# Kernel optimization log

Hardware: AMD Instinct MI355X
Metric: run time of the kernel (lower is better)

Reference implementation:

```python
import jax, jax.numpy as jnp
import numpy as np

TOPK = 13
NUM_CLASSES = 80
ALPHA = 1.0
BETA = 3.0
EPS = 1e-9
K_NEAR = 4
N_BINS = 36  # theta bins: arange(0, 360, 10)


def _dist_max_per_bin(anc_points, gt_pts):
    """gt_pts: (bs,nm,360,2), anc_points: (na,2) -> (bs,nm,na,36) ray targets."""
    d = gt_pts[:, :, None, :, :] - anc_points[None, None, :, None, :]  # (bs,nm,na,360,2)
    dist = jnp.sqrt(jnp.sum(d * d, axis=-1))                           # (bs,nm,na,360)
    ang = jnp.rad2deg(jnp.arctan2(d[..., 1], d[..., 0])) % 360.0       # (bs,nm,na,360)
    theta = jnp.arange(0, 360, 360 // N_BINS).astype(ang.dtype)        # (36,)

    def per_theta(th):
        diff = jnp.abs(ang - th)
        diff = jnp.where(diff > 180.0, 360.0 - diff, diff)
        neg_v, idx = jax.lax.top_k(-diff, K_NEAR)   # 4 nearest-angle contour pts
        val = -neg_v
        dk = jnp.take_along_axis(dist, idx, axis=-1)
        dk = jnp.where(jnp.min(val, axis=-1, keepdims=True) > 3.0, 1e-6, dk)
        return jnp.max(dk, axis=-1)                 # (bs,nm,na)

    dm = jax.lax.map(per_theta, theta)              # (36,bs,nm,na); chunked to bound memory
    return jnp.maximum(jnp.moveaxis(dm, 0, -1), 1e-6)


def _mask_iou(target, pred):
    l_max = jnp.maximum(target, pred)
    l_min = jnp.maximum(jnp.minimum(target, pred), 1e-6)
    return jnp.sum(l_min, -1) / jnp.sum(l_max, -1)


def _forward(pd_scores, pd_bboxes, anc_points, gt_labels, gt_bboxes, mask_gt, gt_coor):
    bs, na, nc = pd_scores.shape
    nm = gt_bboxes.shape[1]
    gl = gt_labels[..., 0]            # (bs,nm) int
    mgt = mask_gt[..., 0]             # (bs,nm) float
    gt_pts = gt_coor.reshape(bs, nm, 360, 2)

    # select_candidates_in_gts: anchor center strictly inside gt box
    lt, rb = gt_bboxes[..., :2], gt_bboxes[..., 2:]
    deltas = jnp.concatenate([anc_points[None, None] - lt[:, :, None],
                              rb[:, :, None] - anc_points[None, None]], axis=-1)
    mask_in_gts = (jnp.min(deltas, -1) > 1e-9).astype(pd_scores.dtype)  # (bs,nm,na)
    mask_sel = (mask_in_gts * mgt[:, :, None]) > 0

    # get_box_metrics_polar (dense over (bs,nm,na) instead of boolean-mask select)
    dist_max = _dist_max_per_bin(anc_points, gt_pts)                    # (bs,nm,na,36)
    overlaps = jnp.where(mask_sel, _mask_iou(dist_max, pd_bboxes[:, None]), 0.0)
    bbox_scores = jnp.take_along_axis(jnp.swapaxes(pd_scores, 1, 2), gl[:, :, None], axis=1)
    bbox_scores = jnp.where(mask_sel, bbox_scores, 0.0)
    align_metric = (bbox_scores ** ALPHA) * (overlaps ** BETA)

    # select_topk_candidates
    _, topk_idxs = jax.lax.top_k(align_metric, TOPK)
    topk_idxs = jnp.where(mgt[:, :, None] > 0, topk_idxs, 0)
    count = jnp.sum(jax.nn.one_hot(topk_idxs, na, dtype=align_metric.dtype), axis=-2)
    mask_topk = jnp.where(count > 1, 0.0, count)
    mask_pos = mask_topk * mask_in_gts * mgt[:, :, None]

    # select_highest_overlaps
    fg = jnp.sum(mask_pos, -2)                                          # (bs,na)
    multi = fg[:, None, :] > 1
    is_max = jnp.moveaxis(jax.nn.one_hot(jnp.argmax(overlaps, 1), nm, dtype=mask_pos.dtype), -1, 1)
    mask_pos = jnp.where(multi, is_max, mask_pos)
    fg_mask = jnp.sum(mask_pos, -2)
    target_gt_idx = jnp.argmax(mask_pos, -2)                            # (bs,na)

    # per-positive ray-distance targets + polar centerness (dense, masked)
    mask_pos_b = mask_pos > 0
    gt_dist = jnp.where(mask_pos_b[..., None], dist_max, 0.0)           # (bs,nm,na,36)
    cent = jnp.sqrt(jnp.min(dist_max, -1) / jnp.max(dist_max, -1))
    centerness_gt = jnp.where(mask_pos_b, cent, 0.0)                    # (bs,nm,na)

    # get_targets
    target_labels = jnp.maximum(jnp.take_along_axis(gl, target_gt_idx, axis=1), 0)
    target_bboxes = jnp.take_along_axis(gt_bboxes, target_gt_idx[..., None], axis=1)
    target_scores = jax.nn.one_hot(target_labels, NUM_CLASSES, dtype=pd_scores.dtype)
    target_scores = jnp.where((fg_mask > 0)[..., None], target_scores, 0.0)

    am = align_metric * mask_pos
    pos_align = jnp.max(am, -1, keepdims=True)
    pos_ov = jnp.max(overlaps * mask_pos, -1, keepdims=True)
    norm_align = jnp.max(am * pos_ov / (pos_align + EPS), -2)[..., None]  # (bs,na,1)
    target_scores = target_scores * norm_align

    return (target_labels, target_bboxes, target_scores, mask_pos_b,
            target_gt_idx, gt_dist, centerness_gt, fg_mask > 0)


def setup_inputs():
    key = jax.random.key(0)
    k = jax.random.split(key, 6)
    bs, nc, nm = 2, 80, 10
    pts, strs = [], []
    for s in (8, 16, 32):  # 640x640 YOLO grid -> 8400 anchors
        n = 640 // s
        yv, xv = np.meshgrid(np.arange(n), np.arange(n), indexing='ij')
        pts.append(np.stack([(xv + 0.5) * s, (yv + 0.5) * s], -1).reshape(-1, 2))
        strs.append(np.full((pts[-1].shape[0], 1), s, dtype=np.float32))
    anc_points = jnp.asarray(np.concatenate(pts).astype(np.float32))
    stride_tensor = jnp.asarray(np.concatenate(strs))
    na = anc_points.shape[0]
    pd_scores = jax.random.uniform(k[0], (bs, na, nc), dtype=jnp.float32)
    pd_bboxes = jax.random.uniform(k[1], (bs, na, 36), dtype=jnp.float32) * 100.0 + 1.0
    gt_labels = jax.random.randint(k[2], (bs, nm, 1), 0, nc)
    ctr = jax.random.uniform(k[3], (bs, nm, 2), dtype=jnp.float32) * 440.0 + 100.0
    wh = jax.random.uniform(k[4], (bs, nm, 2), dtype=jnp.float32) * 140.0 + 40.0
    gt_bboxes = jnp.concatenate([ctr - wh / 2.0, ctr + wh / 2.0], -1)
    th = jnp.arange(360.0) * (jnp.pi / 180.0)
    rad = (jnp.min(wh, -1, keepdims=True) / 2.0) * (0.6 + 0.4 * jax.random.uniform(k[5], (bs, nm, 360), dtype=jnp.float32))
    ray = jnp.stack([jnp.cos(th), jnp.sin(th)], -1)  # (360,2)
    gt_coor = (ctr[:, :, None, :] + rad[..., None] * ray[None, None]).reshape(bs, nm, 720)
    mask_gt = jnp.ones((bs, nm, 1), dtype=jnp.float32).at[1, 7:].set(0.0)
    return dict(pd_scores=pd_scores, pd_bboxes=pd_bboxes, anc_points=anc_points,
                gt_labels=gt_labels, gt_bboxes=gt_bboxes, mask_gt=mask_gt,
                gt_coor=gt_coor, stride_tensor=stride_tensor, ss=640,
                gt_center=ctr, imgsz=640)


def reference(pd_scores, pd_bboxes, anc_points, gt_labels, gt_bboxes, mask_gt, gt_coor, stride_tensor, ss, gt_center, imgsz):
    # ss, gt_center, imgsz, stride_tensor are accepted (as in the torch signature) but unused
    return _forward(pd_scores, pd_bboxes, anc_points, gt_labels, gt_bboxes, mask_gt, gt_coor)
```

## Files before the change

### kernel.cpp

```cpp
#include <hip/hip_runtime.h>

#define BS 2
#define NM 10
#define NA 8400
#define NC 80
#define NBIN 36
#define KTOP 13
#define NRECT (BS*NM*3)
#define WDIST_CAP 16384

typedef unsigned long long ull;

__device__ __forceinline__ void rect_one(int bm, int lv,
    const float* __restrict__ gtb, const float* __restrict__ mgt,
    int& x0, int& y0, int& cx, int& cy, int& cnt, int& n, int& base){
  cnt = 0; x0 = 0; y0 = 0; cx = 0; cy = 0; n = 0; base = 0;
  if (mgt[bm] > 0.f){
    float s = (float)(8 << lv);
    n = 640 >> (3 + lv);
    base = (lv == 0) ? 0 : ((lv == 1) ? 6400 : 8000);
    float lx = gtb[bm*4+0], ly = gtb[bm*4+1];
    float rx = gtb[bm*4+2], ry = gtb[bm*4+3];
    int a0 = (int)ceilf(lx/s - 0.5f); a0 = min(max(a0, 0), n);
    while (a0 > 0   &&  (((a0-1)+0.5f)*s - lx > 1e-9f)) a0--;
    while (a0 < n   && !(((a0  )+0.5f)*s - lx > 1e-9f)) a0++;
    int a1 = (int)floorf(rx/s - 0.5f); a1 = min(max(a1, -1), n-1);
    while (a1 < n-1 &&  (rx - ((a1+1)+0.5f)*s > 1e-9f)) a1++;
    while (a1 >= 0  && !(rx - ((a1  )+0.5f)*s > 1e-9f)) a1--;
    int b0 = (int)ceilf(ly/s - 0.5f); b0 = min(max(b0, 0), n);
    while (b0 > 0   &&  (((b0-1)+0.5f)*s - ly > 1e-9f)) b0--;
    while (b0 < n   && !(((b0  )+0.5f)*s - ly > 1e-9f)) b0++;
    int b1 = (int)floorf(ry/s - 0.5f); b1 = min(max(b1, -1), n-1);
    while (b1 < n-1 &&  (ry - ((b1+1)+0.5f)*s > 1e-9f)) b1++;
    while (b1 >= 0  && !(ry - ((b1  )+0.5f)*s > 1e-9f)) b1--;
    cx = max(0, a1 - a0 + 1);
    cy = max(0, b1 - b0 + 1);
    cnt = cx * cy;
    x0 = a0; y0 = b0;
  }
}

__device__ __forceinline__ void rect_setup(int tid,
    const float* __restrict__ gtb, const float* __restrict__ mgt,
    int* sx0, int* sy0, int* scx, int* scy, int* scum, int* sn, int* sbase){
  if (tid < NRECT){
    int bm = tid/3, lv = tid - bm*3;
    int x0, y0, cx, cy, cnt, n, base;
    rect_one(bm, lv, gtb, mgt, x0, y0, cx, cy, cnt, n, base);
    sx0[tid] = x0; sy0[tid] = y0; scx[tid] = cx; scy[tid] = cy;
    scum[tid] = cnt; sn[tid] = n; sbase[tid] = base;
  }
  __syncthreads();
  if (tid < 64){
    int c = (tid < NRECT) ? scum[tid] : 0;
    int incl = c;
#pragma unroll
    for (int st = 1; st < 64; st <<= 1){
      int o = __shfl_up(incl, st);
      if (tid >= st) incl += o;
    }
    if (tid < NRECT) scum[tid] = incl - c;
    if (tid == NRECT-1) scum[NRECT] = incl;
  }
  __syncthreads();
}

__device__ __forceinline__ int pair_from_p(int p,
    const int* sx0, const int* sy0, const int* scx,
    const int* scum, const int* sn, const int* sbase){
  int lo = 0, hi = NRECT - 1;
  while (lo < hi){ int mid = (lo + hi + 1) >> 1; if (scum[mid] <= p) lo = mid; else hi = mid - 1; }
  int r = lo;
  int idx = p - scum[r];
  int cx = scx[r];
  int yi = idx / cx;
  int xi = idx - yi*cx;
  int a = sbase[r] + (sy0[r] + yi)*sn[r] + (sx0[r] + xi);
  int bm = r/3;
  return bm*NA + a;
}

__device__ __forceinline__ ull shflx_u64(ull v, int off){
  unsigned lo = (unsigned)v, hi = (unsigned)(v >> 32);
  lo = __shfl_xor(lo, off); hi = __shfl_xor(hi, off);
  return ((ull)hi << 32) | lo;
}

__global__ __launch_bounds__(128)
void k_dist(const float* __restrict__ pds, const float* __restrict__ pdb,
            const float* __restrict__ anc, const int* __restrict__ gl,
            const float* __restrict__ gtb, const float* __restrict__ mgt,
            const float* __restrict__ coor,
            float* __restrict__ out, float* __restrict__ wf){
  float* o_labels  = out;
  float* o_bboxes  = o_labels + BS*NA;
  float* o_scores  = o_bboxes + BS*NA*4;
  float* o_maskpos = o_scores + (size_t)BS*NA*NC;
  float* o_gtidx   = o_maskpos + BS*NM*NA;
  float* o_gtdist  = o_gtidx + BS*NA;
  float* o_cent    = o_gtdist + (size_t)BS*NM*NA*NBIN;
  float* o_fg      = o_cent + BS*NM*NA;

  float* w_align = wf + 16;
  float* w_ovl   = w_align + BS*NM*NA;
  float* w_dist  = w_ovl + BS*NM*NA;

  __shared__ int sx0[NRECT], sy0[NRECT], scx[NRECT], scy[NRECT], scum[NRECT+1], sn[NRECT], sbase[NRECT];
  __shared__ float4 s_ad[360];
  __shared__ int s_cnt[NBIN], s_off[NBIN+1], s_cur[NBIN];
  __shared__ int s_fbl[NBIN];
  __shared__ int s_nfb;

  int tid = threadIdx.x;
  int lane = tid & 63, wave = tid >> 6;

  rect_setup(tid, gtb, mgt, sx0, sy0, scx, scy, scum, sn, sbase);
  int total = scum[NRECT];

  {
    int gtid = blockIdx.x*128 + tid, gsz = gridDim.x*128;
    float4 z4 = make_float4(0.f,0.f,0.f,0.f);
    float4* zs = (float4*)o_scores;
    for (int i = gtid; i < (BS*NA*NC)/4; i += gsz) zs[i] = z4;
    float4* zg = (float4*)o_gtdist;
    for (int i = gtid; i < (BS*NM*NA*NBIN)/4; i += gsz) zg[i] = z4;
    float4* zc = (float4*)o_cent;
    for (int i = gtid; i < (BS*NM*NA)/4; i += gsz) zc[i] = z4;
    float4* zm = (float4*)o_maskpos;
    for (int i = gtid; i < (BS*NM*NA)/4; i += gsz) zm[i] = z4;
    if (gtid < 16) wf[gtid] = 0.f;
    for (int t = gtid; t < BS*NA; t += gsz){
      int b = t / NA;
      o_gtidx[t] = 0.f;
      o_fg[t] = 0.f;
      int lbl = gl[b*NM]; if (lbl < 0) lbl = 0;
      o_labels[t] = (float)lbl;
      const float* bx = gtb + (b*NM)*4;
      ((float4*)o_bboxes)[t] = make_float4(bx[0], bx[1], bx[2], bx[3]);
    }
    for (int row = gtid; row < BS*NM*NA; row += gsz){
      int bm = row / NA;
      int a  = row - bm*NA;
      int lv = (a < 6400) ? 0 : ((a < 8000) ? 1 : 2);
      int ai = a - ((lv == 0) ? 0 : ((lv == 1) ? 6400 : 8000));
      int r = bm*3 + lv;
      bool inrect = false;
      if (scx[r] > 0 && scy[r] > 0){
        int n = sn[r];
        int y = ai / n, x = ai - y*n;
        inrect = (x >= sx0[r] && x < sx0[r]+scx[r] &&
                  y >= sy0[r] && y < sy0[r]+scy[r]);
      }
      if (!inrect) w_ovl[row] = 0.f;
    }
  }

  if (tid < NBIN) s_cnt[tid] = 0;
  if (tid == 0) s_nfb = 0;
  __syncthreads();

  for (int p = blockIdx.x; p < total; p += gridDim.x){
    int t = pair_from_p(p, sx0, sy0, scx, scum, sn, sbase);
    int a = t % NA; int bm = t / NA; int b = bm / NM;
    float ax = anc[2*a], ay = anc[2*a+1];
    const float2* cc2 = (const float2*)(coor + bm*720);

    float pr = 0.f, sc = 0.f;
    if (wave == 0){
      if (lane < NBIN) pr = pdb[((size_t)b*NA + a)*NBIN + lane];
      int cls = gl[bm];
      sc = pds[((size_t)b*NA + a)*NC + cls];
    }

    float anR[3], diR[3]; int buR[3];
#pragma unroll
    for (int r = 0; r < 3; r++){
      int i = tid + r*128;
      buR[r] = -1;
      if (i < 360){
        float2 cxy = cc2[i];
        float dx = cxy.x - ax;
        float dy = cxy.y - ay;
        diR[r] = sqrtf(dx*dx + dy*dy);
        float an = atan2f(dy, dx) * 57.29577951308232f;
        if (an < 0.f) an += 360.f;
        anR[r] = an;
        int bu = min((int)(an * 0.1f), NBIN-1);
        buR[r] = bu;
        atomicAdd(&s_cnt[bu], 1);
      }
    }
    __syncthreads();

    if (wave == 0){
      int c = (lane < NBIN) ? s_cnt[lane] : 0;
      int incl = c;
#pragma unroll
      for (int st = 1; st < 64; st <<= 1){
        int o = __shfl_up(incl, st);
        if (lane >= st) incl += o;
      }
      if (lane < NBIN){ s_off[lane+1] = incl; s_cur[lane] = incl - c; }
      if (lane == 0) s_off[0] = 0;
    }
    __syncthreads();

    if (tid < NBIN) s_cnt[tid] = 0;
#pragma unroll
    for (int r = 0; r < 3; r++){
      if (buR[r] >= 0){
        int pos = atomicAdd(&s_cur[buR[r]], 1);
        s_ad[pos] = make_float4(anR[r], diR[r], (float)(tid + r*128), 0.f);
      }
    }
    __syncthreads();

#define EVALJ(J, TH) { \
      float4 ad = s_ad[J]; \
      unsigned int ixv = (unsigned int)(int)ad.z; \
      float df = fabsf(ad.x - (TH)); \
      df = fminf(df, 360.f - df); \
      ull key = ((ull)__float_as_uint(df) << 32) | ixv; \
      if (key < k3){ \
        k3 = key; d3 = ad.y; \
        if (k3 < k2){ ull tk=k2; k2=k3; k3=tk; float td=d2; d2=d3; d3=td; } \
        if (k2 < k1){ ull tk=k1; k1=k2; k2=tk; float td=d1; d1=d2; d2=td; } \
        if (k1 < k0){ ull tk=k0; k0=k1; k1=tk; float td=d0; d0=d1; d1=td; } \
      } }

    if (wave == 0){
      float dfin = 1e-6f;
      bool act = (lane < NBIN);
      bool need_fb = false;
      if (act){
        float th = (float)(lane*10);
        int r0s, r0e, r1s, r1e;
        if (lane == 0)      { r0s = s_off[35]; r0e = s_off[36]; r1s = 0; r1e = s_off[2]; }
        else if (lane == 35){ r0s = s_off[34]; r0e = s_off[36]; r1s = 0; r1e = s_off[1]; }
        else                { r0s = s_off[lane-1]; r0e = s_off[lane+2]; r1s = 0; r1e = 0; }
        ull k0,k1,k2,k3; float d0,d1,d2,d3;
        k0=k1=k2=k3=~0ull; d0=d1=d2=d3=0.f;
        for (int j = r0s; j < r0e; j++) EVALJ(j, th)
        for (int j = r1s; j < r1e; j++) EVALJ(j, th)
        float v0m = __uint_as_float((unsigned)(k0 >> 32));
        float d4v = __uint_as_float((unsigned)(k3 >> 32));
        if (!(v0m <= 3.0f)){
          dfin = 1e-6f;
        } else if (!(d4v <= 9.99f)){
          int fi = atomicAdd(&s_nfb, 1);
          s_fbl[fi] = lane;
          need_fb = true;
        } else {
          dfin = fmaxf(fmaxf(fmaxf(d0,d1),fmaxf(d2,d3)), 1e-6f);
        }
      }
      int nfb = s_nfb;
      for (int f = 0; f < nfb; f++){
        int fb = s_fbl[f];
        float th = (float)(fb*10);
        ull k0,k1,k2,k3; float d0,d1,d2,d3;
        k0=k1=k2=k3=~0ull; d0=d1=d2=d3=0.f;
        for (int j = lane; j < 360; j += 64){
          EVALJ(j, th)
        }
        ull hk = k0; float hd = d0; int hp = 0;
        float dmax = 0.f;
#pragma unroll
        for (int r = 0; r < 4; r++){
          ull mk = hk; float md = hd;
#pragma unroll
          for (int off = 1; off < 64; off <<= 1){
            ull ok = shflx_u64(mk, off);
            float od = __shfl_xor(md, off);
            if (ok < mk){ mk = ok; md = od; }
          }
          if (hk == mk){
            hp++;
            hk = (hp==1)? k1 : (hp==2)? k2 : (hp==3)? k3 : ~0ull;
            hd = (hp==1)? d1 : (hp==2)? d2 : (hp==3)? d3 : 0.f;
          }
          dmax = fmaxf(dmax, md);
        }
        if (lane == fb && need_fb) dfin = fmaxf(dmax, 1e-6f);
      }
      if (lane == 0) s_nfb = 0;

      float sum_min = 0.f, sum_max = 0.f;
      if (act){
        if (p < WDIST_CAP) w_dist[(size_t)p*NBIN + lane] = dfin;
        sum_max = fmaxf(dfin, pr);
        sum_min = fmaxf(fminf(dfin, pr), 1e-6f);
      }
      for (int off = 32; off > 0; off >>= 1){
        sum_min += __shfl_down(sum_min, off);
        sum_max += __shfl_down(sum_max, off);
      }
      if (lane == 0){
        float ov = sum_min / sum_max;
        w_align[t] = sc * ov * ov * ov;
        w_ovl[t]   = ov;
      }
    }
#undef EVALJ
    __syncthreads();
  }
}

__global__ __launch_bounds__(256)
void k_tail(const float* __restrict__ gtb, const float* __restrict__ mgt,
            const float* __restrict__ w_align, const float* __restrict__ w_ovl,
            const float* __restrict__ w_dist, const int* __restrict__ gl,
            float* __restrict__ o_labels, float* __restrict__ o_bboxes,
            float* __restrict__ o_maskpos, float* __restrict__ o_gtidx,
            float* __restrict__ o_fg,
            float* __restrict__ o_gtdist, float* __restrict__ o_cent,
            float* __restrict__ o_scores,
            int* __restrict__ w_sel, int* __restrict__ done){
  __shared__ int sx0[NRECT], sy0[NRECT], scx[NRECT], scy[NRECT], scum[NRECT+1], sn[NRECT], sbase[NRECT];
  __shared__ float sv[256*KTOP];
  __shared__ int   si[256*KTOP];
  __shared__ float wv4[4];
  __shared__ int   wi4[4];
  __shared__ int   sel[BS*NM*KTOP];
  __shared__ unsigned paB[BS*NM], poB[BS*NM];
  __shared__ int fcnt;
  __shared__ int   fT[BS*NM*KTOP];
  __shared__ int   fA[BS*NM*KTOP];
  __shared__ int   fL[BS*NM*KTOP];
  __shared__ float fV[BS*NM*KTOP];
  __shared__ int sLast;

  int tid = threadIdx.x;
  int lane = tid & 63, wave = tid >> 6;

  rect_setup(tid, gtb, mgt, sx0, sy0, scx, scy, scum, sn, sbase);

  int bm = blockIdx.x;
  {
    const float* al = w_align + (size_t)bm*NA;
    int pbase = scum[bm*3], pm1 = scum[bm*3+1], pm2 = scum[bm*3+2], pend = scum[bm*3+3];

    float v[KTOP]; int ix[KTOP];
#pragma unroll
    for (int j = 0; j < KTOP; j++){ v[j] = -1.f; ix[j] = 0x7fffffff; }
    for (int p = pbase + tid; p < pend; p += 256){
      int r = bm*3 + ((p >= pm1) + (p >= pm2));
      int idx = p - scum[r];
      int cx = scx[r];
      int yi = idx / cx;
      int xi = idx - yi*cx;
      int a = sbase[r] + (sy0[r] + yi)*sn[r] + (sx0[r] + xi);
      float x = al[a];
      if (x > v[KTOP-1]){
        v[KTOP-1] = x; ix[KTOP-1] = a;
#pragma unroll
        for (int j = KTOP-1; j > 0; j--){
          if (v[j] > v[j-1]){
            float tv = v[j-1]; v[j-1] = v[j]; v[j] = tv;
            int   ti = ix[j-1]; ix[j-1] = ix[j]; ix[j] = ti;
          }
        }
      }
    }
#pragma unroll
    for (int j = 0; j < KTOP; j++){ sv[tid*KTOP+j] = v[j]; si[tid*KTOP+j] = ix[j]; }

    int head = 0;
    for (int r = 0; r < KTOP; r++){
      float cv = sv[tid*KTOP + head];
      int   ci = si[tid*KTOP + head];
      float rv = cv; int ri = ci;
      for (int off = 32; off > 0; off >>= 1){
        float ov = __shfl_down(rv, off);
        int   oi = __shfl_down(ri, off);
        if (ov > rv || (ov == rv && oi < ri)){ rv = ov; ri = oi; }
      }
      if (lane == 0){ wv4[wave] = rv; wi4[wave] = ri; }
      __syncthreads();
      float Wv = wv4[0]; int Wi = wi4[0];
#pragma unroll
      for (int w = 1; w < 4; w++){
        float ov = wv4[w]; int oi = wi4[w];
        if (ov > Wv || (ov == Wv && oi < Wi)){ Wv = ov; Wi = oi; }
      }
      if (ci == Wi && head < KTOP-1) head++;
      if (tid == 0)
        __hip_atomic_store(&w_sel[bm*KTOP + r], (Wv > 0.f) ? Wi : -1,
                           __ATOMIC_RELAXED, __HIP_MEMORY_SCOPE_AGENT);
      __syncthreads();
    }
  }

  if (tid == 0){
    __threadfence();
    int old = __hip_atomic_fetch_add(done, 1, __ATOMIC_ACQ_REL, __HIP_MEMORY_SCOPE_AGENT);
    sLast = (old == BS*NM - 1) ? 1 : 0;
  }
  __syncthreads();
  if (!sLast) return;

  for (int s = tid; s < BS*NM*KTOP; s += 256)
    sel[s] = __hip_atomic_load(&w_sel[s], __ATOMIC_RELAXED, __HIP_MEMORY_SCOPE_AGENT);
  if (tid < BS*NM){ paB[tid] = 0u; poB[tid] = 0u; }
  if (tid == 0) fcnt = 0;
  __syncthreads();

  for (int s = tid; s < BS*NM*KTOP; s += 256){
    int a = sel[s];
    if (a >= 0){
      int sbm = s / KTOP;
      int b   = sbm / NM;
      int s0 = b*NM*KTOP;
      int cnt = 0, minS = 1 << 30;
      for (int s2 = s0; s2 < s0 + NM*KTOP; s2++){
        if (sel[s2] == a){ cnt++; if (s2 < minS) minS = s2; }
      }
      if (s == minS){
        int bi = sbm - b*NM;
        if (cnt > 1){
          float bv = -1.f; bi = 0;
#pragma unroll
          for (int mm = 0; mm < NM; mm++){
            float vv = w_ovl[((size_t)(b*NM+mm))*NA + a];
            if (vv > bv){ bv = vv; bi = mm; }
          }
        }
        int bmw = b*NM + bi;
        int ta  = b*NA + a;
        o_maskpos[(size_t)bmw*NA + a] = 1.f;
        o_gtidx[ta] = (float)bi;
        o_fg[ta] = 1.f;
        int lbl = gl[bmw]; if (lbl < 0) lbl = 0;
        o_labels[ta] = (float)lbl;
        const float* bx = gtb + bmw*4;
        ((float4*)o_bboxes)[ta] = make_float4(bx[0], bx[1], bx[2], bx[3]);
        float av  = w_align[(size_t)bmw*NA + a];
        float ovv = w_ovl[(size_t)bmw*NA + a];
        atomicMax(&paB[bmw], __float_as_uint(av));
        atomicMax(&poB[bmw], __float_as_uint(ovv));
        int j = atomicAdd(&fcnt, 1);
        fT[j] = bmw*NA + a; fA[j] = ta; fL[j] = lbl; fV[j] = av;
      }
    }
  }
  __syncthreads();

  int nf = fcnt;
  for (int j = tid; j < nf; j += 256){
    int tf = fT[j];
    int a = tf % NA; int bmw = tf / NA;
    int lv = (a < 6400) ? 0 : ((a < 8000) ? 1 : 2);
    int ai = a - ((lv == 0) ? 0 : ((lv == 1) ? 6400 : 8000));
    int r = bmw*3 + lv;
    int n = sn[r];
    int y = ai / n, x = ai - y*n;
    int p = scum[r] + (y - sy0[r])*scx[r] + (x - sx0[r]);
    const float4* src = (const float4*)(w_dist + (size_t)p*NBIN);
    float4* dst = (float4*)(o_gtdist + (size_t)tf*NBIN);
    float vmin = 1e30f, vmax = 0.f;
#pragma unroll
    for (int q = 0; q < 9; q++){
      float4 v4 = src[q];
      dst[q] = v4;
      vmin = fminf(vmin, fminf(fminf(v4.x, v4.y), fminf(v4.z, v4.w)));
      vmax = fmaxf(vmax, fmaxf(fmaxf(v4.x, v4.y), fmaxf(v4.z, v4.w)));
    }
    o_cent[tf] = sqrtf(vmin / vmax);
    float paf = __uint_as_float(paB[bmw]);
    float pof = __uint_as_float(poB[bmw]);
    o_scores[(size_t)fA[j]*NC + fL[j]] = fV[j] * pof / (paf + 1e-9f);
  }
}

extern "C" void kernel_launch(void* const* d_in, const int* in_sizes, int n_in,
                              void* d_out, int out_size, void* d_ws, size_t ws_size,
                              hipStream_t stream){
  const float* pds  = (const float*)d_in[0];
  const float* pdb  = (const float*)d_in[1];
  const float* anc  = (const float*)d_in[2];
  const int*   gl   = (const int*)  d_in[3];
  const float* gtb  = (const float*)d_in[4];
  const float* mgt  = (const float*)d_in[5];
  const float* coor = (const float*)d_in[6];

  float* out = (float*)d_out;
  float* o_labels  = out;
  float* o_bboxes  = o_labels + BS*NA;
  float* o_scores  = o_bboxes + BS*NA*4;
  float* o_maskpos = o_scores + (size_t)BS*NA*NC;
  float* o_gtidx   = o_maskpos + BS*NM*NA;
  float* o_gtdist  = o_gtidx + BS*NA;
  float* o_cent    = o_gtdist + (size_t)BS*NM*NA*NBIN;
  float* o_fg      = o_cent + BS*NM*NA;

  float* wf      = (float*)d_ws;
  int*   done    = (int*)d_ws;
  float* w_align = wf + 16;
  float* w_ovl   = w_align + BS*NM*NA;
  float* w_dist  = w_ovl + BS*NM*NA;
  int*   w_sel   = (int*)(w_dist + (size_t)WDIST_CAP*NBIN);

  k_dist<<<4096, 128, 0, stream>>>(pds, pdb, anc, gl, gtb, mgt, coor, out, wf);
  k_tail<<<BS*NM, 256, 0, stream>>>(gtb, mgt, w_align, w_ovl, w_dist, gl,
                                    o_labels, o_bboxes, o_maskpos, o_gtidx, o_fg,
                                    o_gtdist, o_cent, o_scores, w_sel, done);
}
```

Before: 164.2 us.

## Split per-bin angular top-4 search across two threads and raise grid size

The per-bin nearest-angle top-4 search, previously done by 36 lanes of wave 0, is now split across 72 threads (two per bin), each scanning alternate candidates and merging the two partial top-4 lists with an xor-1 shuffle. Results go to a shared array with an extra block barrier before wave 0 handles fallbacks and the IoU reduction. The grid is enlarged from 4096 to 4608 blocks. This shortens the serial scan per anchor pair at the cost of an added __syncthreads and shuffle-merge work.

Measured after the change: 155.9 us. 5.0% less time.

```diff
diff --git a/kernel.cpp b/kernel.cpp
--- a/kernel.cpp
+++ b/kernel.cpp
@@ -108,6 +108,7 @@
   __shared__ int sx0[NRECT], sy0[NRECT], scx[NRECT], scy[NRECT], scum[NRECT+1], sn[NRECT], sbase[NRECT];
   __shared__ float4 s_ad[360];
   __shared__ int s_cnt[NBIN], s_off[NBIN+1], s_cur[NBIN];
+  __shared__ float s_res[NBIN];
   __shared__ int s_fbl[NBIN];
   __shared__ int s_nfb;
 
@@ -159,6 +160,9 @@
   if (tid == 0) s_nfb = 0;
   __syncthreads();
 
+  int bin2 = tid >> 1;
+  int slot2 = tid & 1;
+
   for (int p = blockIdx.x; p < total; p += gridDim.x){
     int t = pair_from_p(p, sx0, sy0, scx, scum, sn, sbase);
     int a = t % NA; int bm = t / NA; int b = bm / NM;
@@ -228,32 +232,44 @@
         if (k1 < k0){ ull tk=k0; k0=k1; k1=tk; float td=d0; d0=d1; d1=td; } \
       } }
 
-    if (wave == 0){
-      float dfin = 1e-6f;
-      bool act = (lane < NBIN);
-      bool need_fb = false;
-      if (act){
-        float th = (float)(lane*10);
-        int r0s, r0e, r1s, r1e;
-        if (lane == 0)      { r0s = s_off[35]; r0e = s_off[36]; r1s = 0; r1e = s_off[2]; }
-        else if (lane == 35){ r0s = s_off[34]; r0e = s_off[36]; r1s = 0; r1e = s_off[1]; }
-        else                { r0s = s_off[lane-1]; r0e = s_off[lane+2]; r1s = 0; r1e = 0; }
-        ull k0,k1,k2,k3; float d0,d1,d2,d3;
-        k0=k1=k2=k3=~0ull; d0=d1=d2=d3=0.f;
-        for (int j = r0s; j < r0e; j++) EVALJ(j, th)
-        for (int j = r1s; j < r1e; j++) EVALJ(j, th)
-        float v0m = __uint_as_float((unsigned)(k0 >> 32));
-        float d4v = __uint_as_float((unsigned)(k3 >> 32));
+    if (bin2 < NBIN){
+      float th = (float)(bin2*10);
+      int r0s, r0e, r1s, r1e;
+      if (bin2 == 0)      { r0s = s_off[35]; r0e = s_off[36]; r1s = 0; r1e = s_off[2]; }
+      else if (bin2 == 35){ r0s = s_off[34]; r0e = s_off[36]; r1s = 0; r1e = s_off[1]; }
+      else                { r0s = s_off[bin2-1]; r0e = s_off[bin2+2]; r1s = 0; r1e = 0; }
+      int L0 = r0e - r0s, L = L0 + (r1e - r1s);
+      ull k0,k1,k2,k3; float d0,d1,d2,d3;
+      k0=k1=k2=k3=~0ull; d0=d1=d2=d3=0.f;
+      for (int w = slot2; w < L; w += 2){
+        int j = (w < L0) ? (r0s + w) : (r1s + w - L0);
+        EVALJ(j, th)
+      }
+      float v0m = 0.f, d4v = 0.f, dmax = 0.f;
+#pragma unroll
+      for (int r = 0; r < 4; r++){
+        ull mk = k0; float md = d0;
+        ull ok = shflx_u64(mk, 1); float od = __shfl_xor(md, 1);
+        if (ok < mk){ mk = ok; md = od; }
+        if (r == 0) v0m = __uint_as_float((unsigned)(mk >> 32));
+        if (r == 3) d4v = __uint_as_float((unsigned)(mk >> 32));
+        dmax = fmaxf(dmax, md);
+        if (k0 == mk){ k0=k1; d0=d1; k1=k2; d1=d2; k2=k3; d2=d3; k3=~0ull; d3=0.f; }
+      }
+      if (slot2 == 0){
         if (!(v0m <= 3.0f)){
-          dfin = 1e-6f;
+          s_res[bin2] = 1e-6f;
         } else if (!(d4v <= 9.99f)){
           int fi = atomicAdd(&s_nfb, 1);
-          s_fbl[fi] = lane;
-          need_fb = true;
+          s_fbl[fi] = bin2;
         } else {
-          dfin = fmaxf(fmaxf(fmaxf(d0,d1),fmaxf(d2,d3)), 1e-6f);
+          s_res[bin2] = fmaxf(dmax, 1e-6f);
         }
       }
+    }
+    __syncthreads();
+
+    if (wave == 0){
       int nfb = s_nfb;
       for (int f = 0; f < nfb; f++){
         int fb = s_fbl[f];
@@ -281,12 +297,13 @@
           }
           dmax = fmaxf(dmax, md);
         }
-        if (lane == fb && need_fb) dfin = fmaxf(dmax, 1e-6f);
+        if (lane == 0) s_res[fb] = fmaxf(dmax, 1e-6f);
       }
       if (lane == 0) s_nfb = 0;
 
       float sum_min = 0.f, sum_max = 0.f;
-      if (act){
+      if (lane < NBIN){
+        float dfin = s_res[lane];
         if (p < WDIST_CAP) w_dist[(size_t)p*NBIN + lane] = dfin;
         sum_max = fmaxf(dfin, pr);
         sum_min = fmaxf(fminf(dfin, pr), 1e-6f);
@@ -500,7 +517,7 @@
   float* w_dist  = w_ovl + BS*NM*NA;
   int*   w_sel   = (int*)(w_dist + (size_t)WDIST_CAP*NBIN);
 
-  k_dist<<<4096, 128, 0, stream>>>(pds, pdb, anc, gl, gtb, mgt, coor, out, wf);
+  k_dist<<<4608, 128, 0, stream>>>(pds, pdb, anc, gl, gtb, mgt, coor, out, wf);
   k_tail<<<BS*NM, 256, 0, stream>>>(gtb, mgt, w_align, w_ovl, w_dist, gl,
                                     o_labels, o_bboxes, o_maskpos, o_gtidx, o_fg,
                                     o_gtdist, o_cent, o_scores, w_sel, done);
```
